# Performance work log

Hardware: AMD Instinct MI355X
Metric: run time of the kernel (lower is better)

## Reference

```python
import jax, jax.numpy as jnp
import numpy as np

BS, BT, DIM = 32, 1024, 512
NEG_MASK = -1000000.0  # masked_fill value for b/i scores
NEG_SPAN = -1000.0     # lower-triangle fill for span matrix


def setup_inputs() -> dict:
    key = jax.random.key(0)
    ks = jax.random.split(key, 6)
    s = 1.0 / np.sqrt(DIM)  # xavier-ish scale
    return {
        "x": jax.random.normal(ks[0], (BS, DIM), jnp.float32),
        "sen_vecs": jax.random.normal(ks[1], (BS, BT, DIM), jnp.float32),
        "sen_mask": jnp.ones((BS, BT), jnp.int32),
        "Wb": jax.random.normal(ks[2], (DIM, DIM), jnp.float32) * s,
        "bb": jnp.zeros((DIM,), jnp.float32),
        "Wi": jax.random.normal(ks[3], (DIM, DIM), jnp.float32) * s,
        "bi": jnp.zeros((DIM,), jnp.float32),
        "Wo": jax.random.normal(ks[4], (DIM, DIM), jnp.float32) * s,
        "bo": jnp.zeros((DIM,), jnp.float32),
    }


def reference(x, sen_vecs, sen_mask, Wb, bb, Wi, bi, Wo, bo):
    def proj_scores(W, b):
        # torch Linear: sen_vecs @ W.T + b, then dot with x -> [bs, bt]
        h = jnp.einsum('btd,ed->bte', sen_vecs, W) + b
        return jnp.einsum('bte,be->bt', h, x)

    m0 = (sen_mask == 0)
    sb = jnp.where(m0, NEG_MASK, proj_scores(Wb, bb))  # [bs,bt]
    si = jnp.where(m0, NEG_MASK, proj_scores(Wi, bi))
    so = jnp.where(m0, 0.0, proj_scores(Wo, bo))

    # per-step logsumexp over the 3 BIO labels; the CRF-style recursions
    # f[t] = lse(f[t-1] + bio[t-1]) collapse to cumsums since f[t-1] is scalar.
    lse = jax.nn.logsumexp(jnp.stack([sb, si, so], axis=-1), axis=-1)  # [bs,bt]
    z = jnp.zeros((sb.shape[0], 1), sb.dtype)
    fwd = jnp.concatenate([z, jnp.cumsum(lse, axis=1)], axis=1)                      # [bs,bt+1]
    bwd = jnp.concatenate([jnp.flip(jnp.cumsum(jnp.flip(lse, 1), 1), 1), z], axis=1)  # [bs,bt+1]
    full = fwd[:, -1:]

    # prefix sums of scores_i: Ci[t] = sum(si[:t]); sum(si[s:e]) = Ci[e]-Ci[s]
    Ci = jnp.concatenate([z, jnp.cumsum(si, axis=1)], axis=1)  # [bs,bt+1]

    A = sb + fwd[:, :-1] - Ci[:, :-1] - full   # indexed by span start s
    B = Ci[:, :-1] + bwd[:, 1:] + so           # indexed by span end e
    span = A[:, :, None] + B[:, None, :]       # [bs, bt, bt], rows=s, cols=e
    tri = jnp.triu(jnp.ones((sb.shape[1], sb.shape[1]), bool))  # e >= s
    return jnp.where(tri[None], span, jnp.asarray(NEG_SPAN, span.dtype))
```

## Files before the change

kernel.cpp:

```cpp
#include <hip/hip_runtime.h>
#include <math.h>


#define BS 32
#define BT 1024
#define DIM 512
#define NEG_MASK -1000000.0f
#define NEG_SPAN -1000.0f

__global__ __launch_bounds__(256) void k1_proj(
    const float* __restrict__ x,
    const float* __restrict__ Wb, const float* __restrict__ bb,
    const float* __restrict__ Wi, const float* __restrict__ bi,
    const float* __restrict__ Wo, const float* __restrict__ bo,
    float* __restrict__ Y, float* __restrict__ C)
{
    const int w = blockIdx.y;
    const float* __restrict__ W    = (w == 0) ? Wb : (w == 1) ? Wi : Wo;
    const float* __restrict__ bias = (w == 0) ? bb : (w == 1) ? bi : bo;
    const int tid = threadIdx.x;

    if (blockIdx.x == 8) {
        const int v = tid >> 6, l = tid & 63;
        for (int b = v; b < BS; b += 4) {
            float acc = 0.f;
            for (int e = l; e < DIM; e += 64) acc += bias[e] * x[b * DIM + e];
            #pragma unroll
            for (int o = 32; o >= 1; o >>= 1) acc += __shfl_xor(acc, o);
            if (l == 0) C[w * BS + b] = acc;
        }
        return;
    }

    __shared__ float xs[BS * DIM];
    for (int k = tid; k < BS * DIM; k += 256) xs[k] = x[k];
    __syncthreads();

    const int d0 = blockIdx.x * 64;
    const int dt = tid & 63, bg = tid >> 6;
    const int d  = d0 + dt;

    float acc[8];
    #pragma unroll
    for (int i = 0; i < 8; i++) acc[i] = 0.f;
    for (int e = 0; e < DIM; e++) {
        const float wv = W[e * DIM + d];
        #pragma unroll
        for (int i = 0; i < 8; i++)
            acc[i] += wv * xs[(bg * 8 + i) * DIM + e];
    }
    #pragma unroll
    for (int i = 0; i < 8; i++)
        Y[w * BS * DIM + (bg * 8 + i) * DIM + d] = acc[i];
}

__global__ __launch_bounds__(256) void k2a_scores(
    const float* __restrict__ sv, const int* __restrict__ mask,
    const float* __restrict__ Y, const float* __restrict__ C,
    float* __restrict__ SB, float* __restrict__ SI, float* __restrict__ SO,
    float* __restrict__ LSE)
{
    __shared__ float ys[3 * DIM];
    const int blk = blockIdx.x;
    const int b   = blk >> 8;
    const int t0  = (blk & 255) * 4;
    const int tid = threadIdx.x;

    for (int k = tid; k < 3 * DIM; k += 256) {
        const int w = k >> 9, d = k & (DIM - 1);
        ys[k] = Y[w * BS * DIM + b * DIM + d];
    }
    __syncthreads();

    const int v = tid >> 6, l = tid & 63;
    const int t = t0 + v;

    const float4* __restrict__ yb4 = (const float4*)(ys);
    const float4* __restrict__ yi4 = (const float4*)(ys + DIM);
    const float4* __restrict__ yo4 = (const float4*)(ys + 2 * DIM);
    const float4* __restrict__ svp =
        (const float4*)(sv + (size_t)(b * BT + t) * DIM);

    const float4 s1 = svp[l];
    const float4 s2 = svp[64 + l];

    float4 y1, y2;
    y1 = yb4[l]; y2 = yb4[64 + l];
    float aB = s1.x*y1.x + s1.y*y1.y + s1.z*y1.z + s1.w*y1.w
             + s2.x*y2.x + s2.y*y2.y + s2.z*y2.z + s2.w*y2.w;
    y1 = yi4[l]; y2 = yi4[64 + l];
    float aI = s1.x*y1.x + s1.y*y1.y + s1.z*y1.z + s1.w*y1.w
             + s2.x*y2.x + s2.y*y2.y + s2.z*y2.z + s2.w*y2.w;
    y1 = yo4[l]; y2 = yo4[64 + l];
    float aO = s1.x*y1.x + s1.y*y1.y + s1.z*y1.z + s1.w*y1.w
             + s2.x*y2.x + s2.y*y2.y + s2.z*y2.z + s2.w*y2.w;

    #pragma unroll
    for (int o = 32; o >= 1; o >>= 1) {
        aB += __shfl_xor(aB, o);
        aI += __shfl_xor(aI, o);
        aO += __shfl_xor(aO, o);
    }

    if (l == 0) {
        float sb = aB + C[0 * BS + b];
        float si = aI + C[1 * BS + b];
        float so = aO + C[2 * BS + b];
        if (mask[b * BT + t] == 0) { sb = NEG_MASK; si = NEG_MASK; so = 0.f; }
        const float m   = fmaxf(sb, fmaxf(si, so));
        const float lse = m + logf(expf(sb - m) + expf(si - m) + expf(so - m));
        const int idx = b * BT + t;
        SB[idx] = sb; SI[idx] = si; SO[idx] = so; LSE[idx] = lse;
    }
}

__global__ __launch_bounds__(1024) void k2b_scan(
    const float* __restrict__ SB, const float* __restrict__ SI,
    const float* __restrict__ SO, const float* __restrict__ LSE,
    float* __restrict__ A, float* __restrict__ Bv)
{
    __shared__ float sL[BT], sS[BT];
    const int b = blockIdx.x, t = threadIdx.x;
    const float l0 = LSE[b * BT + t];
    const float s0 = SI[b * BT + t];
    sL[t] = l0; sS[t] = s0;
    __syncthreads();

    for (int off = 1; off < BT; off <<= 1) {
        float a = 0.f, c = 0.f;
        if (t >= off) { a = sL[t - off]; c = sS[t - off]; }
        __syncthreads();
        if (t >= off) { sL[t] += a; sS[t] += c; }
        __syncthreads();
    }

    const float total = sL[BT - 1];
    const float pl = sL[t] - l0;
    const float ps = sS[t] - s0;
    A [b * BT + t] = SB[b * BT + t] + pl - ps - total;
    Bv[b * BT + t] = ps + (total - sL[t]) + SO[b * BT + t];
}

__global__ __launch_bounds__(256) void k3_span(
    const float* __restrict__ A, const float* __restrict__ Bv,
    float4* __restrict__ out)
{
    const int idx = blockIdx.x * 256 + threadIdx.x;
    const int b  = idx >> 18;
    const int r  = idx & 0x3FFFF;
    const int i  = r >> 8;
    const int j4 = r & 255;

    const float a = A[b * BT + i];
    const float4 bb4 = ((const float4*)(Bv + b * BT))[j4];
    const int j = j4 * 4;
    float4 o;
    o.x = (j     >= i) ? a + bb4.x : NEG_SPAN;
    o.y = (j + 1 >= i) ? a + bb4.y : NEG_SPAN;
    o.z = (j + 2 >= i) ? a + bb4.z : NEG_SPAN;
    o.w = (j + 3 >= i) ? a + bb4.w : NEG_SPAN;
    out[idx] = o;
}

extern "C" void kernel_launch(void* const* d_in, const int* in_sizes, int n_in,
                              void* d_out, int out_size, void* d_ws, size_t ws_size,
                              hipStream_t stream) {
    const float* x   = (const float*)d_in[0];
    const float* sv  = (const float*)d_in[1];
    const int*   msk = (const int*)  d_in[2];
    const float* Wb  = (const float*)d_in[3];
    const float* bb  = (const float*)d_in[4];
    const float* Wi  = (const float*)d_in[5];
    const float* bi  = (const float*)d_in[6];
    const float* Wo  = (const float*)d_in[7];
    const float* bo  = (const float*)d_in[8];

    float* ws = (float*)d_ws;
    float* Y   = ws;
    float* C   = ws + 49152;
    float* SB  = ws + 49664;
    float* SI  = SB + BS * BT;
    float* SO  = SI + BS * BT;
    float* LSE = SO + BS * BT;
    float* A   = LSE + BS * BT;
    float* Bv  = A + BS * BT;

    k1_proj  <<<dim3(9, 3), 256, 0, stream>>>(x, Wb, bb, Wi, bi, Wo, bo, Y, C);
    k2a_scores<<<BS * 256, 256, 0, stream>>>(sv, msk, Y, C, SB, SI, SO, LSE);
    k2b_scan <<<BS, 1024, 0, stream>>>(SB, SI, SO, LSE, A, Bv);
    k3_span  <<<32768, 256, 0, stream>>>(A, Bv, (float4*)d_out);
}
```

Baseline: 272.8 us.

## Split projection K-dim across blocks, batch two rows per wave, nontemporal streaming

The projection kernel now splits the reduction dimension into 4 chunks across a new grid axis, so it runs 96 blocks instead of 24 and needs less shared memory per block. The partial results are summed when the scores kernel loads them. The scores kernel handles two timesteps per wave, reusing the projected vectors held in registers and halving the block count. Both the sen_vecs loads and the large span output store become nontemporal. The cost is extra partial-sum traffic and a workspace layout change.

```diff
diff --git a/kernel.cpp b/kernel.cpp
--- a/kernel.cpp
+++ b/kernel.cpp
@@ -5,22 +5,28 @@
 #define BS 32
 #define BT 1024
 #define DIM 512
+#define ECH 4
+#define EC  (DIM / ECH)
 #define NEG_MASK -1000000.0f
 #define NEG_SPAN -1000.0f
+
+typedef float f4 __attribute__((ext_vector_type(4)));
 
 __global__ __launch_bounds__(256) void k1_proj(
     const float* __restrict__ x,
     const float* __restrict__ Wb, const float* __restrict__ bb,
     const float* __restrict__ Wi, const float* __restrict__ bi,
     const float* __restrict__ Wo, const float* __restrict__ bo,
-    float* __restrict__ Y, float* __restrict__ C)
+    float* __restrict__ Yp, float* __restrict__ C)
 {
     const int w = blockIdx.y;
+    const int z = blockIdx.z;
     const float* __restrict__ W    = (w == 0) ? Wb : (w == 1) ? Wi : Wo;
     const float* __restrict__ bias = (w == 0) ? bb : (w == 1) ? bi : bo;
     const int tid = threadIdx.x;
 
     if (blockIdx.x == 8) {
+        if (z != 0) return;
         const int v = tid >> 6, l = tid & 63;
         for (int b = v; b < BS; b += 4) {
             float acc = 0.f;
@@ -32,8 +38,12 @@
         return;
     }
 
-    __shared__ float xs[BS * DIM];
-    for (int k = tid; k < BS * DIM; k += 256) xs[k] = x[k];
+    __shared__ float xs[BS * EC];
+    const int e0 = z * EC;
+    for (int k = tid; k < BS * EC; k += 256) {
+        const int b = k >> 7, e = k & (EC - 1);
+        xs[k] = x[b * DIM + e0 + e];
+    }
     __syncthreads();
 
     const int d0 = blockIdx.x * 64;
@@ -43,74 +53,96 @@
     float acc[8];
     #pragma unroll
     for (int i = 0; i < 8; i++) acc[i] = 0.f;
-    for (int e = 0; e < DIM; e++) {
-        const float wv = W[e * DIM + d];
+    for (int e = 0; e < EC; e++) {
+        const float wv = W[(e0 + e) * DIM + d];
         #pragma unroll
         for (int i = 0; i < 8; i++)
-            acc[i] += wv * xs[(bg * 8 + i) * DIM + e];
+            acc[i] += wv * xs[(bg * 8 + i) * EC + e];
     }
     #pragma unroll
     for (int i = 0; i < 8; i++)
-        Y[w * BS * DIM + (bg * 8 + i) * DIM + d] = acc[i];
+        Yp[((z * 3 + w) * BS + bg * 8 + i) * DIM + d] = acc[i];
 }
 
 __global__ __launch_bounds__(256) void k2a_scores(
     const float* __restrict__ sv, const int* __restrict__ mask,
-    const float* __restrict__ Y, const float* __restrict__ C,
+    const float* __restrict__ Yp, const float* __restrict__ C,
     float* __restrict__ SB, float* __restrict__ SI, float* __restrict__ SO,
     float* __restrict__ LSE)
 {
     __shared__ float ys[3 * DIM];
     const int blk = blockIdx.x;
-    const int b   = blk >> 8;
-    const int t0  = (blk & 255) * 4;
+    const int b   = blk >> 7;
+    const int t0  = (blk & 127) * 8;
     const int tid = threadIdx.x;
 
     for (int k = tid; k < 3 * DIM; k += 256) {
         const int w = k >> 9, d = k & (DIM - 1);
-        ys[k] = Y[w * BS * DIM + b * DIM + d];
+        float s = 0.f;
+        #pragma unroll
+        for (int zz = 0; zz < ECH; zz++)
+            s += Yp[((zz * 3 + w) * BS + b) * DIM + d];
+        ys[k] = s;
     }
     __syncthreads();
 
     const int v = tid >> 6, l = tid & 63;
-    const int t = t0 + v;
-
-    const float4* __restrict__ yb4 = (const float4*)(ys);
-    const float4* __restrict__ yi4 = (const float4*)(ys + DIM);
-    const float4* __restrict__ yo4 = (const float4*)(ys + 2 * DIM);
-    const float4* __restrict__ svp =
-        (const float4*)(sv + (size_t)(b * BT + t) * DIM);
-
-    const float4 s1 = svp[l];
-    const float4 s2 = svp[64 + l];
-
-    float4 y1, y2;
-    y1 = yb4[l]; y2 = yb4[64 + l];
-    float aB = s1.x*y1.x + s1.y*y1.y + s1.z*y1.z + s1.w*y1.w
-             + s2.x*y2.x + s2.y*y2.y + s2.z*y2.z + s2.w*y2.w;
-    y1 = yi4[l]; y2 = yi4[64 + l];
-    float aI = s1.x*y1.x + s1.y*y1.y + s1.z*y1.z + s1.w*y1.w
-             + s2.x*y2.x + s2.y*y2.y + s2.z*y2.z + s2.w*y2.w;
-    y1 = yo4[l]; y2 = yo4[64 + l];
-    float aO = s1.x*y1.x + s1.y*y1.y + s1.z*y1.z + s1.w*y1.w
-             + s2.x*y2.x + s2.y*y2.y + s2.z*y2.z + s2.w*y2.w;
+
+    const f4* __restrict__ yb4 = (const f4*)(ys);
+    const f4* __restrict__ yi4 = (const f4*)(ys + DIM);
+    const f4* __restrict__ yo4 = (const f4*)(ys + 2 * DIM);
+
+    const f4 yb1 = yb4[l], yb2 = yb4[64 + l];
+    const f4 yi1 = yi4[l], yi2 = yi4[64 + l];
+    const f4 yo1 = yo4[l], yo2 = yo4[64 + l];
+
+    const int tA = t0 + v, tB = t0 + v + 4;
+    const f4* __restrict__ svA = (const f4*)(sv + (size_t)(b * BT + tA) * DIM);
+    const f4* __restrict__ svB = (const f4*)(sv + (size_t)(b * BT + tB) * DIM);
+
+    const f4 a1 = __builtin_nontemporal_load(svA + l);
+    const f4 a2 = __builtin_nontemporal_load(svA + 64 + l);
+    const f4 b1 = __builtin_nontemporal_load(svB + l);
+    const f4 b2 = __builtin_nontemporal_load(svB + 64 + l);
+
+    #define DOT(p, q, y1, y2) \
+        (p.x*y1.x + p.y*y1.y + p.z*y1.z + p.w*y1.w + \
+         q.x*y2.x + q.y*y2.y + q.z*y2.z + q.w*y2.w)
+
+    float rAB = DOT(a1, a2, yb1, yb2);
+    float rAI = DOT(a1, a2, yi1, yi2);
+    float rAO = DOT(a1, a2, yo1, yo2);
+    float rBB = DOT(b1, b2, yb1, yb2);
+    float rBI = DOT(b1, b2, yi1, yi2);
+    float rBO = DOT(b1, b2, yo1, yo2);
+    #undef DOT
 
     #pragma unroll
     for (int o = 32; o >= 1; o >>= 1) {
-        aB += __shfl_xor(aB, o);
-        aI += __shfl_xor(aI, o);
-        aO += __shfl_xor(aO, o);
+        rAB += __shfl_xor(rAB, o);
+        rAI += __shfl_xor(rAI, o);
+        rAO += __shfl_xor(rAO, o);
+        rBB += __shfl_xor(rBB, o);
+        rBI += __shfl_xor(rBI, o);
+        rBO += __shfl_xor(rBO, o);
     }
 
     if (l == 0) {
-        float sb = aB + C[0 * BS + b];
-        float si = aI + C[1 * BS + b];
-        float so = aO + C[2 * BS + b];
-        if (mask[b * BT + t] == 0) { sb = NEG_MASK; si = NEG_MASK; so = 0.f; }
-        const float m   = fmaxf(sb, fmaxf(si, so));
-        const float lse = m + logf(expf(sb - m) + expf(si - m) + expf(so - m));
-        const int idx = b * BT + t;
-        SB[idx] = sb; SI[idx] = si; SO[idx] = so; LSE[idx] = lse;
+        const float cb = C[0 * BS + b];
+        const float ci = C[1 * BS + b];
+        const float co = C[2 * BS + b];
+        #pragma unroll
+        for (int r = 0; r < 2; r++) {
+            const int t = r ? tB : tA;
+            float sb = (r ? rBB : rAB) + cb;
+            float si = (r ? rBI : rAI) + ci;
+            float so = (r ? rBO : rAO) + co;
+            if (mask[b * BT + t] == 0) { sb = NEG_MASK; si = NEG_MASK; so = 0.f; }
+            const float m   = fmaxf(sb, fmaxf(si, so));
+            const float lse = m + logf(expf(sb - m) + expf(si - m) + expf(so - m));
+            const int idx = b * BT + t;
+            SB[idx] = sb; SI[idx] = si; SO[idx] = so; LSE[idx] = lse;
+        }
     }
 }
 
@@ -143,7 +175,7 @@
 
 __global__ __launch_bounds__(256) void k3_span(
     const float* __restrict__ A, const float* __restrict__ Bv,
-    float4* __restrict__ out)
+    f4* __restrict__ out)
 {
     const int idx = blockIdx.x * 256 + threadIdx.x;
     const int b  = idx >> 18;
@@ -152,14 +184,14 @@
     const int j4 = r & 255;
 
     const float a = A[b * BT + i];
-    const float4 bb4 = ((const float4*)(Bv + b * BT))[j4];
+    const f4 bb4 = ((const f4*)(Bv + b * BT))[j4];
     const int j = j4 * 4;
-    float4 o;
+    f4 o;
     o.x = (j     >= i) ? a + bb4.x : NEG_SPAN;
     o.y = (j + 1 >= i) ? a + bb4.y : NEG_SPAN;
     o.z = (j + 2 >= i) ? a + bb4.z : NEG_SPAN;
     o.w = (j + 3 >= i) ? a + bb4.w : NEG_SPAN;
-    out[idx] = o;
+    __builtin_nontemporal_store(o, out + idx);
 }
 
 extern "C" void kernel_launch(void* const* d_in, const int* in_sizes, int n_in,
@@ -176,17 +208,17 @@
     const float* bo  = (const float*)d_in[8];
 
     float* ws = (float*)d_ws;
-    float* Y   = ws;
-    float* C   = ws + 49152;
-    float* SB  = ws + 49664;
+    float* Yp  = ws;
+    float* C   = ws + ECH * 3 * BS * DIM;
+    float* SB  = C + 512;
     float* SI  = SB + BS * BT;
     float* SO  = SI + BS * BT;
     float* LSE = SO + BS * BT;
     float* A   = LSE + BS * BT;
     float* Bv  = A + BS * BT;
 
-    k1_proj  <<<dim3(9, 3), 256, 0, stream>>>(x, Wb, bb, Wi, bi, Wo, bo, Y, C);
-    k2a_scores<<<BS * 256, 256, 0, stream>>>(sv, msk, Y, C, SB, SI, SO, LSE);
-    k2b_scan <<<BS, 1024, 0, stream>>>(SB, SI, SO, LSE, A, Bv);
-    k3_span  <<<32768, 256, 0, stream>>>(A, Bv, (float4*)d_out);
-}
+    k1_proj   <<<dim3(9, 3, ECH), 256, 0, stream>>>(x, Wb, bb, Wi, bi, Wo, bo, Yp, C);
+    k2a_scores<<<BS * 128, 256, 0, stream>>>(sv, msk, Yp, C, SB, SI, SO, LSE);
+    k2b_scan  <<<BS, 1024, 0, stream>>>(SB, SI, SO, LSE, A, Bv);
+    k3_span   <<<32768, 256, 0, stream>>>(A, Bv, (f4*)d_out);
+}
```

After: 268.8 us. Within noise of the previous version (-1.5%).
